# Kernel tuning notes

Measured on AMD Instinct MI355X. Metric: run time of the kernel, lower is better.

## Reference

```python
import jax, jax.numpy as jnp
import numpy as np

B = 256          # graphs per batch
NPG = 512        # nodes per data graph
NG = B * NPG     # 131072 data-graph nodes
EG = NG * 8      # 1048576 data-graph edges
NQPG = 16        # nodes per query graph
NQ = B * NQPG    # 4096 query nodes
EQ = NQ * 8      # 32768 query edges
IN, H, L, OUT = 64, 128, 2, 1


def setup_inputs() -> dict:
    key = jax.random.key(0)
    ks = jax.random.split(key, 24)
    # edges constrained within each graph (offset + local index)
    g_off = jnp.repeat(jnp.arange(B, dtype=jnp.int32) * NPG, EG // B)
    q_off = jnp.repeat(jnp.arange(B, dtype=jnp.int32) * NQPG, EQ // B)
    inp = {
        "X": jax.random.normal(ks[0], (NG, IN), jnp.float32),
        "X_q": jax.random.normal(ks[1], (NQ, IN), jnp.float32),
        "g_src": g_off + jax.random.randint(ks[2], (EG,), 0, NPG, jnp.int32),
        "g_dst": g_off + jax.random.randint(ks[3], (EG,), 0, NPG, jnp.int32),
        "g_n2g": jnp.repeat(jnp.arange(B, dtype=jnp.int32), NPG),
        "q_src": q_off + jax.random.randint(ks[4], (EQ,), 0, NQPG, jnp.int32),
        "q_dst": q_off + jax.random.randint(ks[5], (EQ,), 0, NQPG, jnp.int32),
        "q_n2g": jnp.repeat(jnp.arange(B, dtype=jnp.int32), NQPG),
    }
    def lin(k, fi, fo):
        s = 1.0 / np.sqrt(fi)
        return jax.random.uniform(k, (fi, fo), jnp.float32, -s, s)
    inp["Wg"] = lin(ks[6], IN, H); inp["bg"] = jnp.zeros((H,), jnp.float32)
    inp["Wq"] = lin(ks[7], IN, H); inp["bq"] = jnp.zeros((H,), jnp.float32)
    inp["betas_g"] = jnp.ones((L,), jnp.float32)  # AGNN beta, init 1
    inp["betas_q"] = jnp.ones((L,), jnp.float32)
    inp["W1r"] = jnp.stack([lin(jax.random.fold_in(ks[8], l), 2 * H, H) for l in range(L)])
    inp["b1r"] = jnp.zeros((L, H), jnp.float32)
    inp["W2r"] = jnp.stack([lin(jax.random.fold_in(ks[9], l), H, H) for l in range(L)])
    inp["b2r"] = jnp.zeros((L, H), jnp.float32)
    inp["Wp1"] = lin(ks[10], H, H); inp["bp1"] = jnp.zeros((H,), jnp.float32)
    inp["Wp2"] = lin(ks[11], H, OUT); inp["bp2"] = jnp.zeros((OUT,), jnp.float32)
    return inp


def agnn(h, src, dst, beta, n):
    # DGL AGNNConv: edge logit = beta * cos(h_dst, h_src); softmax over in-edges of dst;
    # output_i = sum_j alpha_ij * h_j. Nodes with no in-edges get zeros.
    hn = h * jax.lax.rsqrt(jnp.sum(h * h, -1, keepdims=True) + 1e-24)
    e = beta * jnp.sum(hn[src] * hn[dst], -1)                      # [E]
    m = jax.ops.segment_max(e, dst, num_segments=n)
    m = jnp.where(jnp.isfinite(m), m, 0.0)
    ee = jnp.exp(e - m[dst])
    den = jax.ops.segment_sum(ee, dst, num_segments=n)             # [N]
    num = jax.ops.segment_sum(ee[:, None] * h[src], dst, num_segments=n)
    return jnp.where(den[:, None] > 0, num / jnp.maximum(den, 1e-24)[:, None], 0.0)


def reference(X, X_q, g_src, g_dst, g_n2g, q_src, q_dst, q_n2g,
              Wg, bg, Wq, bq, betas_g, betas_q, W1r, b1r, W2r, b2r,
              Wp1, bp1, Wp2, bp2):
    h_g = X @ Wg + bg              # [NG, H]
    h_q = X_q @ Wq + bq            # [NQ, H]
    for l in range(L):
        h_q = agnn(h_q, q_src, q_dst, betas_q[l], NQ)
        h_q_aggr = jax.ops.segment_sum(h_q, q_n2g, num_segments=B)        # dgl.sum_nodes -> [B, H]
        h_cat = jnp.concatenate([h_g, h_q_aggr[g_n2g]], axis=-1)          # per-node broadcast, [NG, 2H]
        h = agnn(h_cat, g_src, g_dst, betas_g[l], NG)                     # [NG, 2H]
        h_g = jax.nn.relu(h @ W1r[l] + b1r[l]) @ W2r[l] + b2r[l]          # MLP reduce -> [NG, H]
    hg_sum = jax.ops.segment_sum(h_g, g_n2g, num_segments=B)             # sum-pool per graph
    y = jax.nn.relu(hg_sum @ Wp1 + bp1) @ Wp2 + bp2                       # SumPredictor -> [B, OUT]
    return y
```

## Files before the change

kernel.cpp:

```cpp
#include <hip/hip_runtime.h>
#include <stdint.h>

#define B_   256
#define NPG  512
#define NG   131072
#define EPG  4096
#define NQPG 16
#define NQ   4096
#define EQPG 128
#define L_   2
#define HPITCH 136

typedef __attribute__((ext_vector_type(8))) short short8;
typedef __attribute__((ext_vector_type(4))) float floatx4;
typedef __attribute__((ext_vector_type(2))) float float2v;

__device__ inline float bf2f(unsigned short u){
    union { unsigned int i; float f; } x; x.i = ((unsigned int)u) << 16; return x.f;
}
__device__ inline unsigned short f2bf(float f){
    union { float f; unsigned int i; } x; x.f = f;
    unsigned int r = x.i + 0x7fff + ((x.i >> 16) & 1);
    return (unsigned short)(r >> 16);
}
__device__ inline float2v bf2x2(unsigned int u){
    union { unsigned int i; float f; } lo, hi;
    lo.i = u << 16; hi.i = u & 0xffff0000u;
    float2v r; r.x = lo.f; r.y = hi.f; return r;
}
__device__ inline float d2(unsigned int a, unsigned int b, float c){
#if __has_builtin(__builtin_amdgcn_fdot2_f32_bf16)
    typedef __attribute__((ext_vector_type(2))) __bf16 bf16x2;
    union { unsigned int u; bf16x2 v; } xa, xb;
    xa.u = a; xb.u = b;
    return __builtin_amdgcn_fdot2_f32_bf16(xa.v, xb.v, c, false);
#else
    union { unsigned int u; float f; } la, ha, lb, hb;
    la.u = a << 16; ha.u = a & 0xffff0000u;
    lb.u = b << 16; hb.u = b & 0xffff0000u;
    return fmaf(la.f, lb.f, fmaf(ha.f, hb.f, c));
#endif
}
__device__ inline float dot8(uint4 a, uint4 b){
    return d2(a.x,b.x, d2(a.y,b.y, d2(a.z,b.z, d2(a.w,b.w, 0.f))));
}
__device__ inline float dot8q(uint4 a, uint4 b, float c0){
    return d2(a.x,b.x, d2(a.y,b.y, d2(a.z,b.z, d2(a.w,b.w, c0))));
}

#if __has_builtin(__builtin_amdgcn_exp2f)
#define FEXP2(x) __builtin_amdgcn_exp2f(x)
#else
#define FEXP2(x) __expf((x) * 0.6931471805599453f)
#endif
#define LOG2E_ 1.4426950408889634f

__device__ inline float red16dpp(float v){
#if __has_builtin(__builtin_amdgcn_mov_dpp)
    int i;
    i = __builtin_amdgcn_mov_dpp(__float_as_int(v), 0xB1, 0xF, 0xF, true);
    v += __int_as_float(i);
    i = __builtin_amdgcn_mov_dpp(__float_as_int(v), 0x4E, 0xF, 0xF, true);
    v += __int_as_float(i);
    i = __builtin_amdgcn_mov_dpp(__float_as_int(v), 0x141, 0xF, 0xF, true);
    v += __int_as_float(i);
    i = __builtin_amdgcn_mov_dpp(__float_as_int(v), 0x128, 0xF, 0xF, true);
    v += __int_as_float(i);
    return v;
#else
    v += __shfl_xor(v,1); v += __shfl_xor(v,2);
    v += __shfl_xor(v,4); v += __shfl_xor(v,8);
    return v;
#endif
}

__device__ inline void red16dpp4(float& v0, float& v1, float& v2, float& v3){
#if defined(__gfx950__) || defined(__gfx942__) || defined(__gfx90a__)
    asm volatile(
        "s_nop 1\n\t"
        "v_add_f32_dpp %0, %0, %0 quad_perm:[1,0,3,2] row_mask:0xf bank_mask:0xf\n\t"
        "v_add_f32_dpp %1, %1, %1 quad_perm:[1,0,3,2] row_mask:0xf bank_mask:0xf\n\t"
        "v_add_f32_dpp %2, %2, %2 quad_perm:[1,0,3,2] row_mask:0xf bank_mask:0xf\n\t"
        "v_add_f32_dpp %3, %3, %3 quad_perm:[1,0,3,2] row_mask:0xf bank_mask:0xf\n\t"
        "v_add_f32_dpp %0, %0, %0 quad_perm:[2,3,0,1] row_mask:0xf bank_mask:0xf\n\t"
        "v_add_f32_dpp %1, %1, %1 quad_perm:[2,3,0,1] row_mask:0xf bank_mask:0xf\n\t"
        "v_add_f32_dpp %2, %2, %2 quad_perm:[2,3,0,1] row_mask:0xf bank_mask:0xf\n\t"
        "v_add_f32_dpp %3, %3, %3 quad_perm:[2,3,0,1] row_mask:0xf bank_mask:0xf\n\t"
        "v_add_f32_dpp %0, %0, %0 row_half_mirror row_mask:0xf bank_mask:0xf\n\t"
        "v_add_f32_dpp %1, %1, %1 row_half_mirror row_mask:0xf bank_mask:0xf\n\t"
        "v_add_f32_dpp %2, %2, %2 row_half_mirror row_mask:0xf bank_mask:0xf\n\t"
        "v_add_f32_dpp %3, %3, %3 row_half_mirror row_mask:0xf bank_mask:0xf\n\t"
        "v_add_f32_dpp %0, %0, %0 row_ror:8 row_mask:0xf bank_mask:0xf\n\t"
        "v_add_f32_dpp %1, %1, %1 row_ror:8 row_mask:0xf bank_mask:0xf\n\t"
        "v_add_f32_dpp %2, %2, %2 row_ror:8 row_mask:0xf bank_mask:0xf\n\t"
        "v_add_f32_dpp %3, %3, %3 row_ror:8 row_mask:0xf bank_mask:0xf"
        : "+v"(v0), "+v"(v1), "+v"(v2), "+v"(v3));
#else
    v0 = red16dpp(v0); v1 = red16dpp(v1); v2 = red16dpp(v2); v3 = red16dpp(v3);
#endif
}

#define ACCUM8(p0,p1,p2,p3,p4,p5,p6,p7,e,u) do { \
    p0 = fmaf(e, bf2f((unsigned short)((u).x&0xffffu)), p0); \
    p1 = fmaf(e, bf2f((unsigned short)((u).x>>16)),    p1); \
    p2 = fmaf(e, bf2f((unsigned short)((u).y&0xffffu)), p2); \
    p3 = fmaf(e, bf2f((unsigned short)((u).y>>16)),    p3); \
    p4 = fmaf(e, bf2f((unsigned short)((u).z&0xffffu)), p4); \
    p5 = fmaf(e, bf2f((unsigned short)((u).z>>16)),    p5); \
    p6 = fmaf(e, bf2f((unsigned short)((u).w&0xffffu)), p6); \
    p7 = fmaf(e, bf2f((unsigned short)((u).w>>16)),    p7); \
} while(0)

#define SMEM_MEGA 11008
__global__ __launch_bounds__(256) void k_mega(
        const int* __restrict__ g_src, const int* __restrict__ g_dst,
        const float* __restrict__ Wg, const float* __restrict__ W1r,
        const float* __restrict__ W2r,
        unsigned short* __restrict__ WgT, unsigned short* __restrict__ W1aT,
        unsigned short* __restrict__ W2rT,
        unsigned short* __restrict__ csrc_g, int* __restrict__ off_g,
        float* __restrict__ degf, unsigned short* __restrict__ nodeperm,
        const float* __restrict__ X_q,
        const float* __restrict__ Wq, const float* __restrict__ bq,
        const int* __restrict__ q_src, const int* __restrict__ q_dst,
        const float* __restrict__ betas_q,
        float* __restrict__ Qv, float* __restrict__ cg2a,
        const float* __restrict__ X,
        const unsigned short* __restrict__ WgT_in,
        const float* __restrict__ bg,
        unsigned short* __restrict__ h_g, float* __restrict__ nrm2){
    extern __shared__ __align__(16) char smem[];
    int bid = blockIdx.x, t = threadIdx.x;
    if (bid < B_){
        int g = bid, lane = t & 63;
        int* cnt   = (int*)smem;
        int* woff  = (int*)(smem + 2048);
        int* gscan = (int*)(smem + 4096);
        int* dh    = (int*)(smem + 4352);
        int* dhoff = (int*)(smem + 4608);
        for (int idx = g*256 + t; idx < 73728; idx += 65536){
            if (idx < 8192){
                int k = idx >> 7, n = idx & 127; WgT[n*64 + k] = f2bf(Wg[idx]);
            } else if (idx < 40960){
                int i = idx - 8192; int l = i >> 14; int j = i & 16383;
                int k = j>>7, n = j&127;
                W1aT[l*16384 + n*128 + k] = f2bf(W1r[l*32768 + j]);
            } else {
                int i = idx - 40960; int l = i >> 14; int j = i & 16383;
                int k = j>>7, n = j&127;
                W2rT[l*16384 + n*128 + k] = f2bf(W2r[i]);
            }
        }
        int gbase = g*NPG; size_t ebase = (size_t)g*EPG;
        for (int n=t;n<NPG;n+=256) cnt[n]=0;
        if (t<64) dh[t]=0;
        __syncthreads();
        for (int i=t;i<EPG;i+=256){
            int d = g_dst[ebase+i]-gbase;
            atomicAdd(&cnt[d],1);
        }
        __syncthreads();
        if (t < 64){
            int s=0;
            #pragma unroll
            for (int j=0;j<8;j++) s += cnt[t*8+j];
            int v=s;
            #pragma unroll
            for (int o=1;o<64;o<<=1){ int u=__shfl_up(v,o); if (lane>=o) v+=u; }
            gscan[t]=v;
        }
        __syncthreads();
        for (int n=t;n<NPG;n+=256){
            int grp=n>>3; int base = grp?gscan[grp-1]:0;
            for (int j=grp*8;j<n;j++) base+=cnt[j];
            off_g[g*NPG+n]=base; woff[n]=base;
            degf[gbase+n] = cnt[n]>0 ? 1.f : 0.f;
            atomicAdd(&dh[cnt[n] < 63 ? cnt[n] : 63], 1);
        }
        __syncthreads();
        if (t < 64){
            int v = dh[t];
            #pragma unroll
            for (int o=1;o<64;o<<=1){ int u=__shfl_up(v,o); if (lane>=o) v+=u; }
            dhoff[t] = v - dh[t];
        }
        __syncthreads();
        for (int n=t;n<NPG;n+=256){
            int d = cnt[n] < 63 ? cnt[n] : 63;
            int pos = atomicAdd(&dhoff[d],1);
            nodeperm[g*NPG+pos] = (unsigned short)n;
        }
        __syncthreads();
        for (int i=t;i<EPG;i+=256){
            int s = g_src[ebase+i]-gbase;
            int d = g_dst[ebase+i]-gbase;
            int pos = atomicAdd(&woff[d],1);
            csrc_g[ebase+pos]=(unsigned short)s;
        }
    } else if (bid < 2*B_){
        int g = bid - B_, sl = t & 15;
        unsigned short* hqrows = (unsigned short*)smem;
        float* xq              = (float*)(smem + 4352);
        float* eq              = (float*)(smem + 8448);
        unsigned short* srcq   = (unsigned short*)(smem + 8960);
        unsigned short* dstq   = (unsigned short*)(smem + 9216);
        float* invq            = (float*)(smem + 9472);
        float* denq            = (float*)(smem + 9536);
        float* hqa             = (float*)(smem + 9600);
        float* cg2s            = (float*)(smem + 10112);
        unsigned int* emaskw   = (unsigned int*)(smem + 10624);
        float* QaccL           = (float*)(smem + 10880);
        for (int i=t;i<NQPG*64;i+=256) xq[i] = X_q[(size_t)g*NQPG*64 + i];
        if (t < EQPG){
            srcq[t] = (unsigned short)(q_src[(size_t)g*EQPG+t] - g*NQPG);
            dstq[t] = (unsigned short)(q_dst[(size_t)g*EQPG+t] - g*NQPG);
        }
        __syncthreads();
        {
            int r = t >> 4, c0 = sl*8;
            float v[8];
            #pragma unroll
            for (int j=0;j<8;j++) v[j] = bq[c0+j];
            for (int k=0;k<64;k++){
                float x = xq[r*64+k];
                const float* wr = Wq + k*128 + c0;
                #pragma unroll
                for (int j=0;j<8;j++) v[j] = fmaf(x, wr[j], v[j]);
            }
            uint4 uu;
            uu.x = (unsigned int)f2bf(v[0]) | ((unsigned int)f2bf(v[1])<<16);
            uu.y = (unsigned int)f2bf(v[2]) | ((unsigned int)f2bf(v[3])<<16);
            uu.z = (unsigned int)f2bf(v[4]) | ((unsigned int)f2bf(v[5])<<16);
            uu.w = (unsigned int)f2bf(v[6]) | ((unsigned int)f2bf(v[7])<<16);
            *(uint4*)(hqrows + r*HPITCH + sl*8) = uu;
        }
        int qn = t >> 4;
        for (int l=0; l<L_; l++){
            float beta_q = betas_q[l];
            if (t < NQPG) denq[t] = 0.f;
            if (t == 16) QaccL[0] = 0.f;
            if (t >= 32 && t < 96) emaskw[t-32] = 0u;
            if (t >= 128 && t < 256) cg2s[t-128] = 0.f;
            __syncthreads();
            {
                uint4 u = *(const uint4*)(hqrows + qn*HPITCH + sl*8);
                float s = red16dpp(dot8(u,u));
                if (sl==0) invq[qn] = rsqrtf(s + 1e-24f);
            }
            __syncthreads();
            for (int e = qn; e < EQPG; e += 16){
                int s = srcq[e], d = dstq[e];
                uint4 us = *(const uint4*)(hqrows + s*HPITCH + sl*8);
                uint4 ud = *(const uint4*)(hqrows + d*HPITCH + sl*8);
                float v = red16dpp(dot8(us, ud));
                if (sl==0){
                    float ee = __expf(beta_q * v * invq[s] * invq[d]);
                    eq[e] = ee;
                    atomicAdd(&denq[d], ee);
                    atomicOr(&emaskw[d*4 + (e>>5)], 1u << (e & 31));
                }
            }
            __syncthreads();
            uint4 nq; nq.x=0; nq.y=0; nq.z=0; nq.w=0;
            {
                float wsum = denq[qn];
                if (wsum > 0.f){
                    float a0=0,a1=0,a2=0,a3=0,a4=0,a5=0,a6=0,a7=0;
                    #pragma unroll
                    for (int w=0;w<4;w++){
                        unsigned int m = emaskw[qn*4+w];
                        while (m){
                            int b = __ffs(m)-1; m &= m-1;
                            int e = w*32 + b;
                            float wg = eq[e];
                            int s = srcq[e];
                            uint4 u = *(const uint4*)(hqrows + s*HPITCH + sl*8);
                            ACCUM8(a0,a1,a2,a3,a4,a5,a6,a7, wg, u);
                        }
                    }
                    float iw = __frcp_rn(wsum);
                    nq.x = (unsigned int)f2bf(a0*iw) | ((unsigned int)f2bf(a1*iw)<<16);
                    nq.y = (unsigned int)f2bf(a2*iw) | ((unsigned int)f2bf(a3*iw)<<16);
                    nq.z = (unsigned int)f2bf(a4*iw) | ((unsigned int)f2bf(a5*iw)<<16);
                    nq.w = (unsigned int)f2bf(a6*iw) | ((unsigned int)f2bf(a7*iw)<<16);
                }
            }
            __syncthreads();
            *(uint4*)(hqrows + qn*HPITCH + sl*8) = nq;
            __syncthreads();
            if (t < 128){
                float s = 0.f;
                for (int n=0;n<NQPG;n++) s += bf2f(hqrows[n*HPITCH + t]);
                hqa[t] = s;
                float qs = s*s;
                #pragma unroll
                for (int o=1;o<64;o<<=1) qs += __shfl_xor(qs, o);
                if ((t & 63) == 0) atomicAdd(&QaccL[0], qs);
            }
            __syncthreads();
            if (t == 0) Qv[l*B_+g] = QaccL[0];
            {
                int jj = t & 127, kc = t >> 7;
                const float* Wl = W1r + (size_t)l*32768;
                float p = 0.f;
                for (int k = kc*64; k < kc*64+64; k++)
                    p = fmaf(hqa[k], Wl[(size_t)(128+k)*128 + jj], p);
                atomicAdd(&cg2s[jj], p);
            }
            __syncthreads();
            if (t < 128) cg2a[((size_t)l*B_+g)*128 + t] = cg2s[t];
            __syncthreads();
        }
    } else {
        const int K = 64;
        int blk = bid - 2*B_;
        int wave = t >> 6, lane = t & 63;
        int quad = lane >> 4, l16 = lane & 15;
        int wrow = blk*64 + wave*16;
        floatx4 acc[8];
        #pragma unroll
        for (int t8=0;t8<8;t8++){
            #pragma unroll
            for (int r=0;r<4;r++) acc[t8][r]=0.f;
        }
        #pragma unroll
        for (int ks = 0; ks < 2; ks++){
            int koff = ks*32 + quad*8;
            const float* ap = X + (size_t)(wrow+l16)*K + koff;
            short8 a;
            #pragma unroll
            for (int j=0;j<8;j++) a[j] = (short)f2bf(ap[j]);
            #pragma unroll
            for (int t8=0;t8<8;t8++){
                short8 b = *(const short8*)(WgT_in + (size_t)(t8*16+l16)*K + koff);
                acc[t8] = __builtin_amdgcn_mfma_f32_16x16x32_bf16(a, b, acc[t8], 0,0,0);
            }
        }
        float ss[4] = {0.f,0.f,0.f,0.f};
        #pragma unroll
        for (int t8=0;t8<8;t8++){
            int col = t8*16 + l16;
            float bv = bg[col];
            #pragma unroll
            for (int r=0;r<4;r++){
                float v = acc[t8][r] + bv;
                h_g[(size_t)(wrow + quad*4 + r)*128 + col] = f2bf(v);
                ss[r] += v*v;
            }
        }
        #pragma unroll
        for (int r=0;r<4;r++){
            #pragma unroll
            for (int o=1;o<16;o<<=1) ss[r] += __shfl_xor(ss[r], o);
        }
        if (l16==0){
            #pragma unroll
            for (int r=0;r<4;r++) nrm2[wrow + quad*4 + r] = ss[r];
        }
    }
}

#define SMEM_GM 152592
#define CIDX(x) ((x) < je1 ? (x) : je1)
#define ROW(i) (*(const uint4*)(hrows + (i)*HPITCH + sl*8))
#define COMP4(U0,U1,U2,U3,I0,I1,I2,I3,JB) do { \
    float v0 = dot8q(U0, ud, Qs); \
    float v1 = dot8q(U1, ud, Qs); \
    float v2 = dot8q(U2, ud, Qs); \
    float v3 = dot8q(U3, ud, Qs); \
    red16dpp4(v0, v1, v2, v3); \
    float e0 = FEXP2(v0 * I0 * bn); \
    float e1 = FEXP2(v1 * I1 * bn); \
    float e2 = FEXP2(v2 * I2 * bn); \
    float e3 = FEXP2(v3 * I3 * bn); \
    if ((JB)+1 >= jend) e1 = 0.f; \
    if ((JB)+2 >= jend) e2 = 0.f; \
    if ((JB)+3 >= jend) e3 = 0.f; \
    ws += (e0 + e1) + (e2 + e3); \
    ax += e0 * bf2x2(U0.x); ay += e0 * bf2x2(U0.y); \
    az += e0 * bf2x2(U0.z); aw += e0 * bf2x2(U0.w); \
    ax += e1 * bf2x2(U1.x); ay += e1 * bf2x2(U1.y); \
    az += e1 * bf2x2(U1.z); aw += e1 * bf2x2(U1.w); \
    ax += e2 * bf2x2(U2.x); ay += e2 * bf2x2(U2.y); \
    az += e2 * bf2x2(U2.z); aw += e2 * bf2x2(U2.w); \
    ax += e3 * bf2x2(U3.x); ay += e3 * bf2x2(U3.y); \
    az += e3 * bf2x2(U3.z); aw += e3 * bf2x2(U3.w); \
} while(0)
__global__ __launch_bounds__(1024) void k_gm(
        const unsigned short* __restrict__ h_g,
        const float* __restrict__ nrm2g,
        const float* __restrict__ betag_p,
        const float* __restrict__ Qv_l,
        const unsigned short* __restrict__ csrc_g,
        const int* __restrict__ off_g,
        const unsigned short* __restrict__ nodeperm,
        unsigned short* __restrict__ aout,
        const unsigned short* __restrict__ W1t, const float* __restrict__ b1,
        const float* __restrict__ cg2, const unsigned short* __restrict__ W2t,
        const float* __restrict__ b2,
        unsigned short* __restrict__ hg_out, float* __restrict__ nrm2out,
        const float* __restrict__ Wp1, const float* __restrict__ bp1,
        const float* __restrict__ Wp2, const float* __restrict__ bp2,
        float* __restrict__ y){
    extern __shared__ __align__(16) char smem[];
    unsigned short* hrows = (unsigned short*)smem;
    float* inv            = (float*)(smem + 139264);
    unsigned short* ssrc  = (unsigned short*)(smem + 141312);
    int* offc             = (int*)(smem + 149504);
    unsigned short* nprm  = (unsigned short*)(smem + 151556);
    int g = blockIdx.x, t = threadIdx.x;
    int group = t >> 4, sl = t & 15;
    float beta_g = betag_p[0];
    int gbase = g*NPG;
    size_t ebase = (size_t)g*EPG;
    int wave = t>>6, lane = t&63, quad = lane>>4, l16 = lane&15;
    float Q = Qv_l[g];
    for (int i=t; i<8192; i+=1024){
        int row = i >> 4, col = i & 15;
        *(uint4*)(hrows + row*HPITCH + col*8) =
            *(const uint4*)(h_g + (size_t)(gbase+row)*128 + col*8);
    }
    for (int n=t; n<NPG; n+=1024){
        inv[n] = rsqrtf(nrm2g[gbase+n] + Q + 1e-24f);
        nprm[n] = nodeperm[g*NPG+n];
    }
    for (int i=t; i<EPG; i+=1024) ssrc[i] = csrc_g[ebase+i];
    for (int n=t; n<=NPG; n+=1024) offc[n] = (n<NPG) ? off_g[g*NPG+n] : EPG;
    __syncthreads();
    float Qs = Q * 0.0625f;
    for (int idx = group; idx < NPG; idx += 64){
        int n = nprm[idx];
        int o = offc[n];
        int jend = offc[n+1];
        uint4 ov;
        if (jend > o){
            uint4 ud = *(const uint4*)(hrows + n*HPITCH + sl*8);
            float bn = beta_g * inv[n] * LOG2E_;
            float ws = 0.f;
            float2v ax; ax.x=0.f; ax.y=0.f;
            float2v ay = ax, az = ax, aw = ax;
            int je1 = jend - 1;
            int iA0 = ssrc[o];
            int iA1 = ssrc[CIDX(o+1)];
            int iA2 = ssrc[CIDX(o+2)];
            int iA3 = ssrc[CIDX(o+3)];
            uint4 uA0 = ROW(iA0);
            uint4 uA1 = ROW(iA1);
            uint4 uA2 = ROW(iA2);
            uint4 uA3 = ROW(iA3);
            float vA0 = inv[iA0], vA1 = inv[iA1], vA2 = inv[iA2], vA3 = inv[iA3];
            int iB0 = ssrc[CIDX(o+4)];
            int iB1 = ssrc[CIDX(o+5)];
            int iB2 = ssrc[CIDX(o+6)];
            int iB3 = ssrc[CIDX(o+7)];
            int j = o;
            for (;;){
                uint4 uB0 = ROW(iB0);
                uint4 uB1 = ROW(iB1);
                uint4 uB2 = ROW(iB2);
                uint4 uB3 = ROW(iB3);
                float vB0 = inv[iB0], vB1 = inv[iB1], vB2 = inv[iB2], vB3 = inv[iB3];
                iA0 = ssrc[CIDX(j+8)];
                iA1 = ssrc[CIDX(j+9)];
                iA2 = ssrc[CIDX(j+10)];
                iA3 = ssrc[CIDX(j+11)];
                COMP4(uA0,uA1,uA2,uA3, vA0,vA1,vA2,vA3, j);
                j += 4; if (j >= jend) break;
                uA0 = ROW(iA0);
                uA1 = ROW(iA1);
                uA2 = ROW(iA2);
                uA3 = ROW(iA3);
                vA0 = inv[iA0]; vA1 = inv[iA1]; vA2 = inv[iA2]; vA3 = inv[iA3];
                iB0 = ssrc[CIDX(j+8)];
                iB1 = ssrc[CIDX(j+9)];
                iB2 = ssrc[CIDX(j+10)];
                iB3 = ssrc[CIDX(j+11)];
                COMP4(uB0,uB1,uB2,uB3, vB0,vB1,vB2,vB3, j);
                j += 4; if (j >= jend) break;
            }
            float iw = __frcp_rn(ws);
            ov.x = (unsigned int)f2bf(ax.x*iw) | ((unsigned int)f2bf(ax.y*iw)<<16);
            ov.y = (unsigned int)f2bf(ay.x*iw) | ((unsigned int)f2bf(ay.y*iw)<<16);
            ov.z = (unsigned int)f2bf(az.x*iw) | ((unsigned int)f2bf(az.y*iw)<<16);
            ov.w = (unsigned int)f2bf(aw.x*iw) | ((unsigned int)f2bf(aw.y*iw)<<16);
        } else {
            ov.x=0; ov.y=0; ov.z=0; ov.w=0;
        }
        *(uint4*)(aout + (size_t)(gbase+n)*128 + sl*8) = ov;
    }
    __syncthreads();
    unsigned short* W1s = (unsigned short*)smem;
    unsigned short* W2s = W1s + 128*136;
    unsigned short* h1  = W2s + 128*136;
    float* hsum = (float*)(smem + 139264);
    float* red2 = hsum + 128;
    #pragma unroll
    for (int p=0;p<2;p++){
        int flat = p*8192 + t*8;
        int n = flat>>7, k = flat&127;
        *(uint4*)(W1s + n*136 + k) = *(const uint4*)(W1t + n*128 + k);
        *(uint4*)(W2s + n*136 + k) = *(const uint4*)(W2t + n*128 + k);
    }
    __syncthreads();
    const int last = (y != nullptr);
    const float* cg = cg2 + (size_t)g*128;
    float psum[8];
    #pragma unroll
    for (int j=0;j<8;j++) psum[j] = 0.f;
    for (int it=0; it<2; it++){
        int rowb = it*256 + wave*16;
        short8 af[4];
        #pragma unroll
        for (int ks=0;ks<4;ks++)
            af[ks] = *(const short8*)(aout + (size_t)(gbase+rowb+l16)*128 + ks*32 + quad*8);
        floatx4 acc[8];
        #pragma unroll
        for (int t8=0;t8<8;t8++){
            #pragma unroll
            for (int r=0;r<4;r++) acc[t8][r]=0.f;
        }
        #pragma unroll
        for (int ks=0;ks<4;ks++){
            int koff = ks*32 + quad*8;
            #pragma unroll
            for (int t8=0;t8<8;t8++){
                short8 b = *(const short8*)(W1s + (t8*16+l16)*136 + koff);
                acc[t8] = __builtin_amdgcn_mfma_f32_16x16x32_bf16(af[ks], b, acc[t8], 0,0,0);
            }
        }
        int lrow = wave*16;
        #pragma unroll
        for (int t8=0;t8<8;t8++){
            int col = t8*16 + l16;
            float bv = b1[col];
            float cv = cg[col];
            #pragma unroll
            for (int r=0;r<4;r++){
                int row = rowb + quad*4 + r;
                float dgv = (offc[row+1] > offc[row]) ? 1.f : 0.f;
                float v = acc[t8][r] + bv + dgv*cv;
                v = v > 0.f ? v : 0.f;
                h1[(lrow + quad*4 + r)*136 + col] = f2bf(v);
            }
        }
        __syncthreads();
        short8 hf[4];
        #pragma unroll
        for (int ks=0;ks<4;ks++)
            hf[ks] = *(const short8*)(h1 + (lrow+l16)*136 + ks*32 + quad*8);
        floatx4 acc2[8];
        #pragma unroll
        for (int t8=0;t8<8;t8++){
            #pragma unroll
            for (int r=0;r<4;r++) acc2[t8][r]=0.f;
        }
        #pragma unroll
        for (int ks=0;ks<4;ks++){
            int koff = ks*32 + quad*8;
            #pragma unroll
            for (int t8=0;t8<8;t8++){
                short8 b = *(const short8*)(W2s + (t8*16+l16)*136 + koff);
                acc2[t8] = __builtin_amdgcn_mfma_f32_16x16x32_bf16(hf[ks], b, acc2[t8], 0,0,0);
            }
        }
        float ss[4] = {0.f,0.f,0.f,0.f};
        #pragma unroll
        for (int t8=0;t8<8;t8++){
            int col = t8*16 + l16;
            float bv = b2[col];
            #pragma unroll
            for (int r=0;r<4;r++){
                float v = acc2[t8][r] + bv;
                if (last){
                    psum[t8] += v;
                } else {
                    hg_out[(size_t)(gbase + rowb + quad*4 + r)*128 + col] = f2bf(v);
                    ss[r] += v*v;
                }
            }
        }
        if (!last){
            #pragma unroll
            for (int r=0;r<4;r++){
                #pragma unroll
                for (int o=1;o<16;o<<=1) ss[r] += __shfl_xor(ss[r], o);
            }
            if (l16==0){
                #pragma unroll
                for (int r=0;r<4;r++)
                    nrm2out[gbase + rowb + quad*4 + r] = ss[r];
            }
        }
        __syncthreads();
    }
    if (last){
        if (t < 128) hsum[t] = 0.f;
        __syncthreads();
        #pragma unroll
        for (int j=0;j<8;j++){
            psum[j] += __shfl_xor(psum[j], 16);
            psum[j] += __shfl_xor(psum[j], 32);
        }
        if (lane < 16){
            #pragma unroll
            for (int j=0;j<8;j++) atomicAdd(&hsum[j*16 + lane], psum[j]);
        }
        __syncthreads();
        if (t < 128){
            float acc = bp1[t];
            for (int k=0;k<128;k++) acc += hsum[k]*Wp1[k*128+t];
            acc = fmaxf(acc, 0.f);
            red2[t] = acc * Wp2[t];
        }
        __syncthreads();
        for (int s2=64; s2>0; s2>>=1){
            if (t<s2) red2[t]+=red2[t+s2];
            __syncthreads();
        }
        if (t==0) y[g] = red2[0] + bp2[0];
    }
}

extern "C" void kernel_launch(void* const* d_in, const int* in_sizes, int n_in,
                              void* d_out, int out_size, void* d_ws, size_t ws_size,
                              hipStream_t stream) {
    const float* X    = (const float*)d_in[0];
    const float* X_q  = (const float*)d_in[1];
    const int* g_src = (const int*)d_in[2];
    const int* g_dst = (const int*)d_in[3];
    const int* q_src = (const int*)d_in[5];
    const int* q_dst = (const int*)d_in[6];
    const float* Wg   = (const float*)d_in[8];
    const float* bg   = (const float*)d_in[9];
    const float* Wq   = (const float*)d_in[10];
    const float* bq   = (const float*)d_in[11];
    const float* betas_g = (const float*)d_in[12];
    const float* betas_q = (const float*)d_in[13];
    const float* W1r  = (const float*)d_in[14];
    const float* b1r  = (const float*)d_in[15];
    const float* W2r  = (const float*)d_in[16];
    const float* b2r  = (const float*)d_in[17];
    const float* Wp1  = (const float*)d_in[18];
    const float* bp1  = (const float*)d_in[19];
    const float* Wp2  = (const float*)d_in[20];
    const float* bp2  = (const float*)d_in[21];

    uint8_t* w = (uint8_t*)d_ws;
    unsigned short* h_g  = (unsigned short*)w;    w += (size_t)NG*128*2;
    unsigned short* aout = (unsigned short*)w;    w += (size_t)NG*128*2;
    float* nrm2  = (float*)w;                     w += (size_t)NG*4;
    float* degf  = (float*)w;                     w += (size_t)NG*4;
    float* Qv    = (float*)w;                     w += (size_t)L_*B_*4;
    float* cg2a  = (float*)w;                     w += (size_t)L_*B_*128*4;
    unsigned short* WgT   = (unsigned short*)w;   w += 8192*2;
    unsigned short* W1aT  = (unsigned short*)w;   w += 2*16384*2;
    unsigned short* W2rT  = (unsigned short*)w;   w += 2*16384*2;
    unsigned short* csrc_g = (unsigned short*)w;  w += (size_t)B_*EPG*2;
    unsigned short* nodeperm = (unsigned short*)w; w += (size_t)B_*NPG*2;
    int* off_g = (int*)w;                         w += (size_t)B_*NPG*4;

    static bool attr_done = false;
    if (!attr_done){
        hipFuncSetAttribute((const void*)k_gm,
                            hipFuncAttributeMaxDynamicSharedMemorySize, SMEM_GM);
        attr_done = true;
    }

    k_mega<<<2*B_ + NG/64, 256, SMEM_MEGA, stream>>>(
        g_src, g_dst, Wg, W1r, W2r, WgT, W1aT, W2rT,
        csrc_g, off_g, degf, nodeperm,
        X_q, Wq, bq, q_src, q_dst, betas_q, Qv, cg2a,
        X, WgT, bg, h_g, nrm2);
    for (int l=0;l<L_;l++){
        k_gm<<<B_, 1024, SMEM_GM, stream>>>(
            h_g, nrm2, betas_g + l, Qv + l*B_,
            csrc_g, off_g, nodeperm, aout,
            W1aT + l*16384, b1r + l*128, cg2a + (size_t)l*B_*128,
            W2rT + l*16384, b2r + l*128,
            h_g, (l==0) ? nrm2 : nullptr,
            Wp1, bp1, Wp2, bp2,
            (l==L_-1) ? (float*)d_out : nullptr);
    }
}
```

Baseline: 259.0 us.

## Fuse both graph AGNN+MLP layers into one per-graph kernel launch

Merges the two per-layer k_gm launches into a single k_uber2 kernel in which each block loops over both layers for its graph. Edge lists, offsets and the node permutation are loaded into LDS once and reused across layers, and the squared norms for layer 2 stay in shared memory instead of round-tripping through global memory. This removes one launch and the redundant reloads. In exchange, layer-1 writes of h_g to global memory must be visible to the same block when it reads them back for layer 2, and every block now runs longer.

```diff
diff --git a/kernel.cpp b/kernel.cpp
--- a/kernel.cpp
+++ b/kernel.cpp
@@ -386,19 +386,18 @@
     ax += e3 * bf2x2(U3.x); ay += e3 * bf2x2(U3.y); \
     az += e3 * bf2x2(U3.z); aw += e3 * bf2x2(U3.w); \
 } while(0)
-__global__ __launch_bounds__(1024) void k_gm(
-        const unsigned short* __restrict__ h_g,
+__global__ __launch_bounds__(1024) void k_uber2(
+        unsigned short* hbuf,
         const float* __restrict__ nrm2g,
-        const float* __restrict__ betag_p,
-        const float* __restrict__ Qv_l,
+        const float* __restrict__ betas_g,
+        const float* __restrict__ Qv,
         const unsigned short* __restrict__ csrc_g,
         const int* __restrict__ off_g,
         const unsigned short* __restrict__ nodeperm,
         unsigned short* __restrict__ aout,
-        const unsigned short* __restrict__ W1t, const float* __restrict__ b1,
-        const float* __restrict__ cg2, const unsigned short* __restrict__ W2t,
-        const float* __restrict__ b2,
-        unsigned short* __restrict__ hg_out, float* __restrict__ nrm2out,
+        const unsigned short* __restrict__ W1aT, const float* __restrict__ b1r,
+        const float* __restrict__ cg2a,
+        const unsigned short* __restrict__ W2rT, const float* __restrict__ b2r,
         const float* __restrict__ Wp1, const float* __restrict__ bp1,
         const float* __restrict__ Wp2, const float* __restrict__ bp2,
         float* __restrict__ y){
@@ -410,190 +409,201 @@
     unsigned short* nprm  = (unsigned short*)(smem + 151556);
     int g = blockIdx.x, t = threadIdx.x;
     int group = t >> 4, sl = t & 15;
-    float beta_g = betag_p[0];
     int gbase = g*NPG;
     size_t ebase = (size_t)g*EPG;
     int wave = t>>6, lane = t&63, quad = lane>>4, l16 = lane&15;
-    float Q = Qv_l[g];
-    for (int i=t; i<8192; i+=1024){
-        int row = i >> 4, col = i & 15;
-        *(uint4*)(hrows + row*HPITCH + col*8) =
-            *(const uint4*)(h_g + (size_t)(gbase+row)*128 + col*8);
-    }
-    for (int n=t; n<NPG; n+=1024){
-        inv[n] = rsqrtf(nrm2g[gbase+n] + Q + 1e-24f);
-        nprm[n] = nodeperm[g*NPG+n];
-    }
-    for (int i=t; i<EPG; i+=1024) ssrc[i] = csrc_g[ebase+i];
-    for (int n=t; n<=NPG; n+=1024) offc[n] = (n<NPG) ? off_g[g*NPG+n] : EPG;
-    __syncthreads();
-    float Qs = Q * 0.0625f;
-    for (int idx = group; idx < NPG; idx += 64){
-        int n = nprm[idx];
-        int o = offc[n];
-        int jend = offc[n+1];
-        uint4 ov;
-        if (jend > o){
-            uint4 ud = *(const uint4*)(hrows + n*HPITCH + sl*8);
-            float bn = beta_g * inv[n] * LOG2E_;
-            float ws = 0.f;
-            float2v ax; ax.x=0.f; ax.y=0.f;
-            float2v ay = ax, az = ax, aw = ax;
-            int je1 = jend - 1;
-            int iA0 = ssrc[o];
-            int iA1 = ssrc[CIDX(o+1)];
-            int iA2 = ssrc[CIDX(o+2)];
-            int iA3 = ssrc[CIDX(o+3)];
-            uint4 uA0 = ROW(iA0);
-            uint4 uA1 = ROW(iA1);
-            uint4 uA2 = ROW(iA2);
-            uint4 uA3 = ROW(iA3);
-            float vA0 = inv[iA0], vA1 = inv[iA1], vA2 = inv[iA2], vA3 = inv[iA3];
-            int iB0 = ssrc[CIDX(o+4)];
-            int iB1 = ssrc[CIDX(o+5)];
-            int iB2 = ssrc[CIDX(o+6)];
-            int iB3 = ssrc[CIDX(o+7)];
-            int j = o;
-            for (;;){
-                uint4 uB0 = ROW(iB0);
-                uint4 uB1 = ROW(iB1);
-                uint4 uB2 = ROW(iB2);
-                uint4 uB3 = ROW(iB3);
-                float vB0 = inv[iB0], vB1 = inv[iB1], vB2 = inv[iB2], vB3 = inv[iB3];
-                iA0 = ssrc[CIDX(j+8)];
-                iA1 = ssrc[CIDX(j+9)];
-                iA2 = ssrc[CIDX(j+10)];
-                iA3 = ssrc[CIDX(j+11)];
-                COMP4(uA0,uA1,uA2,uA3, vA0,vA1,vA2,vA3, j);
-                j += 4; if (j >= jend) break;
-                uA0 = ROW(iA0);
-                uA1 = ROW(iA1);
-                uA2 = ROW(iA2);
-                uA3 = ROW(iA3);
-                vA0 = inv[iA0]; vA1 = inv[iA1]; vA2 = inv[iA2]; vA3 = inv[iA3];
-                iB0 = ssrc[CIDX(j+8)];
-                iB1 = ssrc[CIDX(j+9)];
-                iB2 = ssrc[CIDX(j+10)];
-                iB3 = ssrc[CIDX(j+11)];
-                COMP4(uB0,uB1,uB2,uB3, vB0,vB1,vB2,vB3, j);
-                j += 4; if (j >= jend) break;
-            }
-            float iw = __frcp_rn(ws);
-            ov.x = (unsigned int)f2bf(ax.x*iw) | ((unsigned int)f2bf(ax.y*iw)<<16);
-            ov.y = (unsigned int)f2bf(ay.x*iw) | ((unsigned int)f2bf(ay.y*iw)<<16);
-            ov.z = (unsigned int)f2bf(az.x*iw) | ((unsigned int)f2bf(az.y*iw)<<16);
-            ov.w = (unsigned int)f2bf(aw.x*iw) | ((unsigned int)f2bf(aw.y*iw)<<16);
-        } else {
-            ov.x=0; ov.y=0; ov.z=0; ov.w=0;
-        }
-        *(uint4*)(aout + (size_t)(gbase+n)*128 + sl*8) = ov;
-    }
-    __syncthreads();
-    unsigned short* W1s = (unsigned short*)smem;
-    unsigned short* W2s = W1s + 128*136;
-    unsigned short* h1  = W2s + 128*136;
-    float* hsum = (float*)(smem + 139264);
-    float* red2 = hsum + 128;
-    #pragma unroll
-    for (int p=0;p<2;p++){
-        int flat = p*8192 + t*8;
-        int n = flat>>7, k = flat&127;
-        *(uint4*)(W1s + n*136 + k) = *(const uint4*)(W1t + n*128 + k);
-        *(uint4*)(W2s + n*136 + k) = *(const uint4*)(W2t + n*128 + k);
-    }
-    __syncthreads();
-    const int last = (y != nullptr);
-    const float* cg = cg2 + (size_t)g*128;
     float psum[8];
     #pragma unroll
     for (int j=0;j<8;j++) psum[j] = 0.f;
-    for (int it=0; it<2; it++){
-        int rowb = it*256 + wave*16;
-        short8 af[4];
+    for (int l=0; l<L_; l++){
+        float Q = Qv[l*B_+g];
+        float beta_g = betas_g[l];
+        for (int i=t; i<8192; i+=1024){
+            int row = i >> 4, col = i & 15;
+            *(uint4*)(hrows + row*HPITCH + col*8) =
+                *(const uint4*)(hbuf + (size_t)(gbase+row)*128 + col*8);
+        }
+        if (l == 0){
+            for (int n=t; n<NPG; n+=1024){
+                inv[n] = rsqrtf(nrm2g[gbase+n] + Q + 1e-24f);
+                nprm[n] = nodeperm[g*NPG+n];
+            }
+            for (int i=t; i<EPG; i+=1024) ssrc[i] = csrc_g[ebase+i];
+            for (int n=t; n<=NPG; n+=1024) offc[n] = (n<NPG) ? off_g[g*NPG+n] : EPG;
+        } else {
+            for (int n=t; n<NPG; n+=1024) inv[n] = rsqrtf(inv[n] + Q + 1e-24f);
+        }
+        __syncthreads();
+        float Qs = Q * 0.0625f;
+        for (int idx = group; idx < NPG; idx += 64){
+            int n = nprm[idx];
+            int o = offc[n];
+            int jend = offc[n+1];
+            uint4 ov;
+            if (jend > o){
+                uint4 ud = *(const uint4*)(hrows + n*HPITCH + sl*8);
+                float bn = beta_g * inv[n] * LOG2E_;
+                float ws = 0.f;
+                float2v ax; ax.x=0.f; ax.y=0.f;
+                float2v ay = ax, az = ax, aw = ax;
+                int je1 = jend - 1;
+                int iA0 = ssrc[o];
+                int iA1 = ssrc[CIDX(o+1)];
+                int iA2 = ssrc[CIDX(o+2)];
+                int iA3 = ssrc[CIDX(o+3)];
+                uint4 uA0 = ROW(iA0);
+                uint4 uA1 = ROW(iA1);
+                uint4 uA2 = ROW(iA2);
+                uint4 uA3 = ROW(iA3);
+                float vA0 = inv[iA0], vA1 = inv[iA1], vA2 = inv[iA2], vA3 = inv[iA3];
+                int iB0 = ssrc[CIDX(o+4)];
+                int iB1 = ssrc[CIDX(o+5)];
+                int iB2 = ssrc[CIDX(o+6)];
+                int iB3 = ssrc[CIDX(o+7)];
+                int j = o;
+                for (;;){
+                    uint4 uB0 = ROW(iB0);
+                    uint4 uB1 = ROW(iB1);
+                    uint4 uB2 = ROW(iB2);
+                    uint4 uB3 = ROW(iB3);
+                    float vB0 = inv[iB0], vB1 = inv[iB1], vB2 = inv[iB2], vB3 = inv[iB3];
+                    iA0 = ssrc[CIDX(j+8)];
+                    iA1 = ssrc[CIDX(j+9)];
+                    iA2 = ssrc[CIDX(j+10)];
+                    iA3 = ssrc[CIDX(j+11)];
+                    COMP4(uA0,uA1,uA2,uA3, vA0,vA1,vA2,vA3, j);
+                    j += 4; if (j >= jend) break;
+                    uA0 = ROW(iA0);
+                    uA1 = ROW(iA1);
+                    uA2 = ROW(iA2);
+                    uA3 = ROW(iA3);
+                    vA0 = inv[iA0]; vA1 = inv[iA1]; vA2 = inv[iA2]; vA3 = inv[iA3];
+                    iB0 = ssrc[CIDX(j+8)];
+                    iB1 = ssrc[CIDX(j+9)];
+                    iB2 = ssrc[CIDX(j+10)];
+                    iB3 = ssrc[CIDX(j+11)];
+                    COMP4(uB0,uB1,uB2,uB3, vB0,vB1,vB2,vB3, j);
+                    j += 4; if (j >= jend) break;
+                }
+                float iw = __frcp_rn(ws);
+                ov.x = (unsigned int)f2bf(ax.x*iw) | ((unsigned int)f2bf(ax.y*iw)<<16);
+                ov.y = (unsigned int)f2bf(ay.x*iw) | ((unsigned int)f2bf(ay.y*iw)<<16);
+                ov.z = (unsigned int)f2bf(az.x*iw) | ((unsigned int)f2bf(az.y*iw)<<16);
+                ov.w = (unsigned int)f2bf(aw.x*iw) | ((unsigned int)f2bf(aw.y*iw)<<16);
+            } else {
+                ov.x=0; ov.y=0; ov.z=0; ov.w=0;
+            }
+            *(uint4*)(aout + (size_t)(gbase+n)*128 + sl*8) = ov;
+        }
+        __syncthreads();
+        unsigned short* W1s = (unsigned short*)smem;
+        unsigned short* W2s = W1s + 128*136;
+        unsigned short* h1  = W2s + 128*136;
+        float* invf = (float*)(smem + 139264);
+        const unsigned short* W1t = W1aT + l*16384;
+        const unsigned short* W2t = W2rT + l*16384;
+        const float* b1 = b1r + l*128;
+        const float* b2 = b2r + l*128;
+        const float* cg = cg2a + ((size_t)l*B_ + g)*128;
         #pragma unroll
-        for (int ks=0;ks<4;ks++)
-            af[ks] = *(const short8*)(aout + (size_t)(gbase+rowb+l16)*128 + ks*32 + quad*8);
-        floatx4 acc[8];
-        #pragma unroll
-        for (int t8=0;t8<8;t8++){
-            #pragma unroll
-            for (int r=0;r<4;r++) acc[t8][r]=0.f;
-        }
-        #pragma unroll
-        for (int ks=0;ks<4;ks++){
-            int koff = ks*32 + quad*8;
+        for (int p=0;p<2;p++){
+            int flat = p*8192 + t*8;
+            int n = flat>>7, k = flat&127;
+            *(uint4*)(W1s + n*136 + k) = *(const uint4*)(W1t + n*128 + k);
+            *(uint4*)(W2s + n*136 + k) = *(const uint4*)(W2t + n*128 + k);
+        }
+        __syncthreads();
+        const int last = (l == L_-1);
+        for (int it=0; it<2; it++){
+            int rowb = it*256 + wave*16;
+            short8 af[4];
+            #pragma unroll
+            for (int ks=0;ks<4;ks++)
+                af[ks] = *(const short8*)(aout + (size_t)(gbase+rowb+l16)*128 + ks*32 + quad*8);
+            floatx4 acc[8];
             #pragma unroll
             for (int t8=0;t8<8;t8++){
-                short8 b = *(const short8*)(W1s + (t8*16+l16)*136 + koff);
-                acc[t8] = __builtin_amdgcn_mfma_f32_16x16x32_bf16(af[ks], b, acc[t8], 0,0,0);
-            }
-        }
-        int lrow = wave*16;
-        #pragma unroll
-        for (int t8=0;t8<8;t8++){
-            int col = t8*16 + l16;
-            float bv = b1[col];
-            float cv = cg[col];
-            #pragma unroll
-            for (int r=0;r<4;r++){
-                int row = rowb + quad*4 + r;
-                float dgv = (offc[row+1] > offc[row]) ? 1.f : 0.f;
-                float v = acc[t8][r] + bv + dgv*cv;
-                v = v > 0.f ? v : 0.f;
-                h1[(lrow + quad*4 + r)*136 + col] = f2bf(v);
-            }
-        }
-        __syncthreads();
-        short8 hf[4];
-        #pragma unroll
-        for (int ks=0;ks<4;ks++)
-            hf[ks] = *(const short8*)(h1 + (lrow+l16)*136 + ks*32 + quad*8);
-        floatx4 acc2[8];
-        #pragma unroll
-        for (int t8=0;t8<8;t8++){
-            #pragma unroll
-            for (int r=0;r<4;r++) acc2[t8][r]=0.f;
-        }
-        #pragma unroll
-        for (int ks=0;ks<4;ks++){
-            int koff = ks*32 + quad*8;
+                #pragma unroll
+                for (int r=0;r<4;r++) acc[t8][r]=0.f;
+            }
+            #pragma unroll
+            for (int ks=0;ks<4;ks++){
+                int koff = ks*32 + quad*8;
+                #pragma unroll
+                for (int t8=0;t8<8;t8++){
+                    short8 b = *(const short8*)(W1s + (t8*16+l16)*136 + koff);
+                    acc[t8] = __builtin_amdgcn_mfma_f32_16x16x32_bf16(af[ks], b, acc[t8], 0,0,0);
+                }
+            }
+            int lrow = wave*16;
             #pragma unroll
             for (int t8=0;t8<8;t8++){
-                short8 b = *(const short8*)(W2s + (t8*16+l16)*136 + koff);
-                acc2[t8] = __builtin_amdgcn_mfma_f32_16x16x32_bf16(hf[ks], b, acc2[t8], 0,0,0);
-            }
-        }
-        float ss[4] = {0.f,0.f,0.f,0.f};
-        #pragma unroll
-        for (int t8=0;t8<8;t8++){
-            int col = t8*16 + l16;
-            float bv = b2[col];
-            #pragma unroll
-            for (int r=0;r<4;r++){
-                float v = acc2[t8][r] + bv;
-                if (last){
-                    psum[t8] += v;
-                } else {
-                    hg_out[(size_t)(gbase + rowb + quad*4 + r)*128 + col] = f2bf(v);
-                    ss[r] += v*v;
-                }
-            }
-        }
-        if (!last){
-            #pragma unroll
-            for (int r=0;r<4;r++){
-                #pragma unroll
-                for (int o=1;o<16;o<<=1) ss[r] += __shfl_xor(ss[r], o);
-            }
-            if (l16==0){
-                #pragma unroll
-                for (int r=0;r<4;r++)
-                    nrm2out[gbase + rowb + quad*4 + r] = ss[r];
-            }
-        }
-        __syncthreads();
+                int col = t8*16 + l16;
+                float bv = b1[col];
+                float cv = cg[col];
+                #pragma unroll
+                for (int r=0;r<4;r++){
+                    int row = rowb + quad*4 + r;
+                    float dgv = (offc[row+1] > offc[row]) ? 1.f : 0.f;
+                    float v = acc[t8][r] + bv + dgv*cv;
+                    v = v > 0.f ? v : 0.f;
+                    h1[(lrow + quad*4 + r)*136 + col] = f2bf(v);
+                }
+            }
+            __syncthreads();
+            short8 hf[4];
+            #pragma unroll
+            for (int ks=0;ks<4;ks++)
+                hf[ks] = *(const short8*)(h1 + (lrow+l16)*136 + ks*32 + quad*8);
+            floatx4 acc2[8];
+            #pragma unroll
+            for (int t8=0;t8<8;t8++){
+                #pragma unroll
+                for (int r=0;r<4;r++) acc2[t8][r]=0.f;
+            }
+            #pragma unroll
+            for (int ks=0;ks<4;ks++){
+                int koff = ks*32 + quad*8;
+                #pragma unroll
+                for (int t8=0;t8<8;t8++){
+                    short8 b = *(const short8*)(W2s + (t8*16+l16)*136 + koff);
+                    acc2[t8] = __builtin_amdgcn_mfma_f32_16x16x32_bf16(hf[ks], b, acc2[t8], 0,0,0);
+                }
+            }
+            float ss[4] = {0.f,0.f,0.f,0.f};
+            #pragma unroll
+            for (int t8=0;t8<8;t8++){
+                int col = t8*16 + l16;
+                float bv = b2[col];
+                #pragma unroll
+                for (int r=0;r<4;r++){
+                    float v = acc2[t8][r] + bv;
+                    if (last){
+                        psum[t8] += v;
+                    } else {
+                        hbuf[(size_t)(gbase + rowb + quad*4 + r)*128 + col] = f2bf(v);
+                        ss[r] += v*v;
+                    }
+                }
+            }
+            if (!last){
+                #pragma unroll
+                for (int r=0;r<4;r++){
+                    #pragma unroll
+                    for (int o=1;o<16;o<<=1) ss[r] += __shfl_xor(ss[r], o);
+                }
+                if (l16==0){
+                    #pragma unroll
+                    for (int r=0;r<4;r++)
+                        invf[rowb + quad*4 + r] = ss[r];
+                }
+            }
+            __syncthreads();
+        }
     }
-    if (last){
+    {
+        float* hsum = (float*)(smem + 139264);
+        float* red2 = hsum + 128;
         if (t < 128) hsum[t] = 0.f;
         __syncthreads();
         #pragma unroll
@@ -661,7 +671,7 @@
 
     static bool attr_done = false;
     if (!attr_done){
-        hipFuncSetAttribute((const void*)k_gm,
+        hipFuncSetAttribute((const void*)k_uber2,
                             hipFuncAttributeMaxDynamicSharedMemorySize, SMEM_GM);
         attr_done = true;
     }
@@ -671,14 +681,8 @@
         csrc_g, off_g, degf, nodeperm,
         X_q, Wq, bq, q_src, q_dst, betas_q, Qv, cg2a,
         X, WgT, bg, h_g, nrm2);
-    for (int l=0;l<L_;l++){
-        k_gm<<<B_, 1024, SMEM_GM, stream>>>(
-            h_g, nrm2, betas_g + l, Qv + l*B_,
-            csrc_g, off_g, nodeperm, aout,
-            W1aT + l*16384, b1r + l*128, cg2a + (size_t)l*B_*128,
-            W2rT + l*16384, b2r + l*128,
-            h_g, (l==0) ? nrm2 : nullptr,
-            Wp1, bp1, Wp2, bp2,
-            (l==L_-1) ? (float*)d_out : nullptr);
-    }
-}
+    k_uber2<<<B_, 1024, SMEM_GM, stream>>>(
+        h_g, nrm2, betas_g, Qv, csrc_g, off_g, nodeperm, aout,
+        W1aT, b1r, cg2a, W2rT, b2r,
+        Wp1, bp1, Wp2, bp2, (float*)d_out);
+}
```

Result: slower. 277.9 us (+7.3%).
